# Optimization experiments

Measured on AMD Instinct MI355X. Metric: run time of the kernel, lower is better.

Reference implementation:

```python
import jax, jax.numpy as jnp
import numpy as np

NHEAD = 8
HEAD_DIM = 32  # per-head dim d; C = NHEAD * HEAD_DIM = 256
NEG_INF = -1e9


def setup_inputs() -> dict:
    key = jax.random.key(0)
    k1, k2, k3, k4, k5 = jax.random.split(key, 5)
    B, L, C = 8, 1024, NHEAD * HEAD_DIM
    query = jax.random.normal(k1, (B, L, C), dtype=jnp.float32)
    key_t = jax.random.normal(k2, (B, L, C), dtype=jnp.float32)
    value = jax.random.normal(k3, (B, L, C), dtype=jnp.float32)
    hard_mask = jax.random.randint(k4, (B, L), 0, 2).astype(bool)
    bias = jax.random.normal(k5, (B, L, L), dtype=jnp.float32)
    return {"query": query, "key": key_t, "value": value,
            "hard_mask": hard_mask, "bias": bias}


def reference(query, key, value, hard_mask, bias):
    # Faithful to the hard-mask path: attention is computed only among
    # active tokens (hard_mask True); inactive positions pass `value` through.
    # Masking inactive KEYS with -inf in the softmax is mathematically
    # identical to the sort/gather/slice/SDPA/scatter-unsort in the original.
    B, L, C = query.shape
    H, D = NHEAD, HEAD_DIM
    scale = 1.0 / jnp.sqrt(jnp.asarray(D, query.dtype))

    def split_heads(t):  # (B, L, C) -> (B, H, L, D)
        return t.reshape(B, L, H, D).transpose(0, 2, 1, 3)

    q, k, v = split_heads(query), split_heads(key), split_heads(value)

    # scores: (B, H, Lq, Lk); bias broadcasts over heads
    scores = jnp.einsum('bhld,bhmd->bhlm', q, k) * scale + bias[:, None, :, :]
    scores = jnp.where(hard_mask[:, None, None, :], scores, NEG_INF)
    attn = jax.nn.softmax(scores, axis=-1)
    out = jnp.einsum('bhlm,bhmd->bhld', attn, v)          # (B, H, L, D)
    out = out.transpose(0, 2, 1, 3).reshape(B, L, C)      # (B, L, C)

    # inactive query positions return the raw value (scatter-back behavior)
    out = jnp.where(hard_mask[:, :, None], out, value)

    # torch.stack over per-item (1, L, C) results -> (B, 1, L, C)
    return out[:, None, :, :]
```

## Files before the change

### kernel.cpp

```cpp
#include <hip/hip_runtime.h>
#include <hip/hip_bf16.h>

#define B_    8
#define H_    8
#define L_    1024
#define D_    32
#define C_    256
#define NK    64
#define PSTR  72

typedef __attribute__((ext_vector_type(8))) short bf16x8;
typedef __attribute__((ext_vector_type(4))) float f32x4;

__device__ inline unsigned short f2bf(float f) {
    union { float f; unsigned int u; } x; x.f = f;
    return (unsigned short)((x.u + 0x7fffu + ((x.u >> 16) & 1u)) >> 16);
}

__device__ inline unsigned int pk_bf16(float lo, float hi) {
    union { __hip_bfloat162 h; unsigned int u; } c;
    c.h = __float22bfloat162_rn(make_float2(lo, hi));
    return c.u;
}

__global__ __launch_bounds__(256) void prep_all(
    const float* __restrict__ k, const float* __restrict__ v,
    const float* __restrict__ bias, const int* __restrict__ mask,
    unsigned short* __restrict__ kfrag, unsigned short* __restrict__ vfrag,
    unsigned short* __restrict__ bfrag)
{
    const int tid = threadIdx.x;
    const int blk = blockIdx.x;
    __shared__ float sKf[64 * 36];
    __shared__ float sVf[64 * 33];
    __shared__ float sMadd[L_];

    if (blk < 1024) {
        const int bh = blk >> 4, c = blk & 15;
        const int b = bh >> 3, h = bh & 7;
        {
            const int row = tid >> 2, seg = tid & 3;
            const size_t src = (size_t)(b * L_ + c * 64 + row) * C_ + h * D_ + seg * 8;
            float4 a = *(const float4*)(k + src);
            float4 d = *(const float4*)(k + src + 4);
            *(float4*)(sKf + row * 36 + seg * 8) = a;
            *(float4*)(sKf + row * 36 + seg * 8 + 4) = d;
            float4 va = *(const float4*)(v + src);
            float4 vd = *(const float4*)(v + src + 4);
            float* vr = sVf + row * 33 + seg * 8;
            vr[0] = va.x; vr[1] = va.y; vr[2] = va.z; vr[3] = va.w;
            vr[4] = vd.x; vr[5] = vd.y; vr[6] = vd.z; vr[7] = vd.w;
        }
        __syncthreads();
        const int ln = tid & 63, u = tid >> 6;
        const int l16 = ln & 15, quad = ln >> 4;
        {
            const float* src = sKf + (u * 16 + l16) * 36 + quad * 8;
            float4 a = *(const float4*)src;
            float4 d = *(const float4*)(src + 4);
            uint4 o = { pk_bf16(a.x, a.y), pk_bf16(a.z, a.w),
                        pk_bf16(d.x, d.y), pk_bf16(d.z, d.w) };
            *(uint4*)(kfrag + (size_t)blk * 2048 + u * 512 + ln * 8) = o;
        }
        {
            const int s2 = u >> 1, nt = u & 1;
            float vals[8];
#pragma unroll
            for (int j = 0; j < 8; ++j)
                vals[j] = sVf[(s2 * 32 + quad * 8 + j) * 33 + nt * 16 + l16];
            uint4 o = { pk_bf16(vals[0], vals[1]), pk_bf16(vals[2], vals[3]),
                        pk_bf16(vals[4], vals[5]), pk_bf16(vals[6], vals[7]) };
            *(uint4*)(vfrag + (size_t)blk * 2048 + s2 * 1024 + nt * 512 + ln * 8) = o;
        }
    } else {
        const int bblk = blk - 1024;
        const int b = bblk >> 6, strip = bblk & 63;
        const int wv = tid >> 6, ln = tid & 63;
        const int l16 = ln & 15, quad = ln >> 4;
        {
            int4 m = ((const int4*)(mask + b * L_))[tid];
            sMadd[tid * 4 + 0] = m.x ? 0.f : -1e9f;
            sMadd[tid * 4 + 1] = m.y ? 0.f : -1e9f;
            sMadd[tid * 4 + 2] = m.z ? 0.f : -1e9f;
            sMadd[tid * 4 + 3] = m.w ? 0.f : -1e9f;
        }
        __syncthreads();
        const float* brow = bias + ((size_t)(b * L_) + strip * 16 + quad * 4) * L_;
        unsigned short* obase = bfrag + (size_t)bblk * 16384;
#pragma unroll
        for (int cc = 0; cc < 4; ++cc) {
            const int c = wv * 4 + cc;
            float vals[16];
#pragma unroll
            for (int nt = 0; nt < 4; ++nt) {
                const int col = c * 64 + nt * 16 + l16;
                const float madd = sMadd[col];
#pragma unroll
                for (int r = 0; r < 4; ++r)
                    vals[nt * 4 + r] = brow[(size_t)r * L_ + col] + madd;
            }
            uint4 o0 = { pk_bf16(vals[0],  vals[1]),  pk_bf16(vals[2],  vals[3]),
                         pk_bf16(vals[4],  vals[5]),  pk_bf16(vals[6],  vals[7]) };
            uint4 o1 = { pk_bf16(vals[8],  vals[9]),  pk_bf16(vals[10], vals[11]),
                         pk_bf16(vals[12], vals[13]), pk_bf16(vals[14], vals[15]) };
            *(uint4*)(obase + c * 1024 +   0 + ln * 8) = o0;
            *(uint4*)(obase + c * 1024 + 512 + ln * 8) = o1;
        }
    }
}

__global__ __launch_bounds__(256, 4) void attn_fa2(
    const float* __restrict__ q,
    const float* __restrict__ v,
    const int*   __restrict__ mask,
    const unsigned short* __restrict__ kfrag,
    const unsigned short* __restrict__ vfrag,
    const unsigned short* __restrict__ bfrag,
    float*       __restrict__ out)
{
    __shared__ __align__(16) unsigned short sP[4][16 * PSTR];

    const int tid  = threadIdx.x;
    const int wv   = tid >> 6;
    const int ln   = tid & 63;
    const int l16  = ln & 15;
    const int quad = ln >> 4;

    const int blk = blockIdx.x;
    const int h   = blk >> 7;
    const int rem = blk & 127;
    const int b   = rem >> 4;
    const int qt  = rem & 15;
    const int strip = qt * 4 + wv;
    const int q0  = strip * 16;
    const int bh  = b * H_ + h;

    const float scale = 0.17677669529663687f;

    bf16x8 qfrag;
    {
        const float* qp = q + ((size_t)(b * L_ + q0 + l16) * C_ + h * D_ + quad * 8);
        float4 a = ((const float4*)qp)[0];
        float4 c = ((const float4*)qp)[1];
        __align__(16) unsigned int u[4] = {
            pk_bf16(a.x * scale, a.y * scale), pk_bf16(a.z * scale, a.w * scale),
            pk_bf16(c.x * scale, c.y * scale), pk_bf16(c.z * scale, c.w * scale)};
        qfrag = *(const bf16x8*)u;
    }

    bf16x8 onesf;
#pragma unroll
    for (int i = 0; i < 8; ++i) onesf[i] = (short)0x3F80;

    const unsigned short* kf_base = kfrag + (size_t)bh * 32768 + ln * 8;
    const unsigned short* vf_base = vfrag + (size_t)bh * 32768 + ln * 8;
    const unsigned short* bm_base = bfrag + (size_t)(b * 64 + strip) * 16384 + ln * 8;
    unsigned short* const sPw = &sP[wv][0];

    f32x4 Oacc[2] = {{0.f,0.f,0.f,0.f},{0.f,0.f,0.f,0.f}};
    f32x4 Lacc    = {0.f,0.f,0.f,0.f};

    bf16x8 kf[4];
    uint4  bm[2];
#pragma unroll
    for (int nt = 0; nt < 4; ++nt)
        kf[nt] = *(const bf16x8*)(kf_base + nt * 512);
    bm[0] = *(const uint4*)(bm_base);
    bm[1] = *(const uint4*)(bm_base + 512);

    for (int c = 0; c < 16; ++c) {
        bf16x8 vf[4];
#pragma unroll
        for (int u2 = 0; u2 < 4; ++u2)
            vf[u2] = *(const bf16x8*)(vf_base + c * 2048 + u2 * 512);

        f32x4 S[4];
#pragma unroll
        for (int nt = 0; nt < 4; ++nt)
            S[nt] = __builtin_amdgcn_mfma_f32_16x16x32_bf16(
                qfrag, kf[nt], (f32x4){0.f,0.f,0.f,0.f}, 0, 0, 0);

        const int cn = (c < 15) ? c + 1 : 15;
        bf16x8 kfN[4];
        uint4  bmN[2];
#pragma unroll
        for (int nt = 0; nt < 4; ++nt)
            kfN[nt] = *(const bf16x8*)(kf_base + cn * 2048 + nt * 512);
        bmN[0] = *(const uint4*)(bm_base + cn * 1024);
        bmN[1] = *(const uint4*)(bm_base + cn * 1024 + 512);

        unsigned short* dst0 = sPw + quad * 4 * PSTR + l16;
#pragma unroll
        for (int nt = 0; nt < 4; ++nt) {
            const unsigned int w0 = ((const unsigned int*)&bm[nt >> 1])[(nt & 1) * 2 + 0];
            const unsigned int w1 = ((const unsigned int*)&bm[nt >> 1])[(nt & 1) * 2 + 1];
            const float b0 = __uint_as_float(w0 << 16);
            const float b1 = __uint_as_float(w0 & 0xffff0000u);
            const float b2 = __uint_as_float(w1 << 16);
            const float b3 = __uint_as_float(w1 & 0xffff0000u);
            const float p0 = __expf(S[nt][0] + b0);
            const float p1 = __expf(S[nt][1] + b1);
            const float p2 = __expf(S[nt][2] + b2);
            const float p3 = __expf(S[nt][3] + b3);
            const unsigned int plo = pk_bf16(p0, p1);
            const unsigned int phi = pk_bf16(p2, p3);
            unsigned short* d = dst0 + nt * 16;
            d[0 * PSTR] = (unsigned short)plo;
            d[1 * PSTR] = (unsigned short)(plo >> 16);
            d[2 * PSTR] = (unsigned short)phi;
            d[3 * PSTR] = (unsigned short)(phi >> 16);
        }

#pragma unroll
        for (int s2 = 0; s2 < 2; ++s2) {
            bf16x8 pf = *(const bf16x8*)(sPw + l16 * PSTR + s2 * 32 + quad * 8);
            Lacc = __builtin_amdgcn_mfma_f32_16x16x32_bf16(pf, onesf, Lacc, 0, 0, 0);
            Oacc[0] = __builtin_amdgcn_mfma_f32_16x16x32_bf16(pf, vf[s2 * 2 + 0], Oacc[0], 0, 0, 0);
            Oacc[1] = __builtin_amdgcn_mfma_f32_16x16x32_bf16(pf, vf[s2 * 2 + 1], Oacc[1], 0, 0, 0);
        }

#pragma unroll
        for (int nt = 0; nt < 4; ++nt) kf[nt] = kfN[nt];
        bm[0] = bmN[0];
        bm[1] = bmN[1];
    }

#pragma unroll
    for (int r = 0; r < 4; ++r) {
        const int qrow = q0 + quad * 4 + r;
        const int active = mask[b * L_ + qrow];
        const float inv = 1.f / Lacc[r];
        const size_t base = (size_t)(b * L_ + qrow) * C_ + h * D_;
#pragma unroll
        for (int nt = 0; nt < 2; ++nt) {
            const size_t idx = base + nt * 16 + l16;
            out[idx] = active ? Oacc[nt][r] * inv : v[idx];
        }
    }
}

#define MQ    64
#define KSTR  48
#define VSTR  72

__global__ __launch_bounds__(256) void masked_attn_mfma(
    const float* __restrict__ q,
    const float* __restrict__ k,
    const float* __restrict__ v,
    const int*   __restrict__ mask,
    const float* __restrict__ bias,
    float*       __restrict__ out)
{
    __shared__ __align__(16) unsigned short sQ[MQ][KSTR];
    __shared__ __align__(16) unsigned short sKt[NK][KSTR];
    __shared__ __align__(16) unsigned short sVt[D_][VSTR];
    __shared__ __align__(16) unsigned short sP2[4][16][VSTR];
    __shared__ float sMadd2[NK];

    const int tid  = threadIdx.x;
    const int wv   = tid >> 6;
    const int ln   = tid & 63;
    const int l16  = ln & 15;
    const int quad = ln >> 4;

    const int blk = blockIdx.x;
    const int h   = blk & 7;
    const int qt  = (blk >> 3) & 15;
    const int b   = blk >> 7;
    const int q0  = qt * MQ;
    const float scale = 0.17677669529663687f;

    {
        const int row = tid >> 2, d0 = (tid & 3) * 8;
        const float* src = q + ((size_t)(b * L_ + q0 + row) * C_ + h * D_ + d0);
        float4 a = ((const float4*)src)[0];
        float4 c = ((const float4*)src)[1];
        __align__(16) unsigned short t8[8] = {
            f2bf(a.x), f2bf(a.y), f2bf(a.z), f2bf(a.w),
            f2bf(c.x), f2bf(c.y), f2bf(c.z), f2bf(c.w)};
        *(int4*)&sQ[row][d0] = *(const int4*)t8;
    }
    __syncthreads();

    const bf16x8 qfrag = *(const bf16x8*)&sQ[wv * 16 + l16][quad * 8];
    f32x4 Oacc[2] = {{0.f,0.f,0.f,0.f},{0.f,0.f,0.f,0.f}};
    float lsum[4] = {0.f, 0.f, 0.f, 0.f};

    for (int j0 = 0; j0 < L_; j0 += NK) {
        __syncthreads();
        {
            const int row = tid >> 2, d0 = (tid & 3) * 8;
            const size_t src = (size_t)(b * L_ + j0 + row) * C_ + h * D_ + d0;
            float4 ka = ((const float4*)(k + src))[0];
            float4 kb = ((const float4*)(k + src))[1];
            __align__(16) unsigned short t8[8] = {
                f2bf(ka.x), f2bf(ka.y), f2bf(ka.z), f2bf(ka.w),
                f2bf(kb.x), f2bf(kb.y), f2bf(kb.z), f2bf(kb.w)};
            *(int4*)&sKt[row][d0] = *(const int4*)t8;

            float4 va = ((const float4*)(v + src))[0];
            float4 vb = ((const float4*)(v + src))[1];
            sVt[d0 + 0][row] = f2bf(va.x);
            sVt[d0 + 1][row] = f2bf(va.y);
            sVt[d0 + 2][row] = f2bf(va.z);
            sVt[d0 + 3][row] = f2bf(va.w);
            sVt[d0 + 4][row] = f2bf(vb.x);
            sVt[d0 + 5][row] = f2bf(vb.y);
            sVt[d0 + 6][row] = f2bf(vb.z);
            sVt[d0 + 7][row] = f2bf(vb.w);
            if (tid < NK) sMadd2[tid] = mask[b * L_ + j0 + tid] ? 0.f : -1e9f;
        }
        __syncthreads();

        bf16x8 kf[4];
#pragma unroll
        for (int nt = 0; nt < 4; ++nt)
            kf[nt] = *(const bf16x8*)&sKt[nt * 16 + l16][quad * 8];

        f32x4 S[4];
#pragma unroll
        for (int nt = 0; nt < 4; ++nt)
            S[nt] = __builtin_amdgcn_mfma_f32_16x16x32_bf16(
                qfrag, kf[nt], (f32x4){0.f,0.f,0.f,0.f}, 0, 0, 0);

        float psum[4] = {0.f, 0.f, 0.f, 0.f};
        const size_t brow0 = (size_t)(b * L_ + q0 + wv * 16 + quad * 4) * L_ + j0;
#pragma unroll
        for (int nt = 0; nt < 4; ++nt) {
            const float madd = sMadd2[nt * 16 + l16];
#pragma unroll
            for (int r = 0; r < 4; ++r) {
                float s = S[nt][r] * scale + bias[brow0 + (size_t)r * L_ + nt * 16 + l16] + madd;
                float p = __expf(s);
                psum[r] += p;
                S[nt][r] = p;
            }
        }
#pragma unroll
        for (int nt = 0; nt < 4; ++nt)
#pragma unroll
            for (int r = 0; r < 4; ++r)
                sP2[wv][quad * 4 + r][nt * 16 + l16] = f2bf(S[nt][r]);
#pragma unroll
        for (int r = 0; r < 4; ++r) {
            float t = psum[r];
            t += __shfl_xor(t, 1);
            t += __shfl_xor(t, 2);
            t += __shfl_xor(t, 4);
            t += __shfl_xor(t, 8);
            lsum[r] += t;
        }
#pragma unroll
        for (int s2 = 0; s2 < 2; ++s2) {
            bf16x8 pf = *(const bf16x8*)&sP2[wv][l16][s2 * 32 + quad * 8];
#pragma unroll
            for (int nt = 0; nt < 2; ++nt) {
                bf16x8 vf = *(const bf16x8*)&sVt[nt * 16 + l16][s2 * 32 + quad * 8];
                Oacc[nt] = __builtin_amdgcn_mfma_f32_16x16x32_bf16(pf, vf, Oacc[nt], 0, 0, 0);
            }
        }
    }
#pragma unroll
    for (int r = 0; r < 4; ++r) {
        const int qg = q0 + wv * 16 + quad * 4 + r;
        const int active = mask[b * L_ + qg];
        const size_t obase = (size_t)(b * L_ + qg) * C_ + h * D_;
        const float inv = 1.f / lsum[r];
#pragma unroll
        for (int nt = 0; nt < 2; ++nt) {
            float val;
            if (active) val = Oacc[nt][r] * inv;
            else        val = v[obase + nt * 16 + l16];
            out[obase + nt * 16 + l16] = val;
        }
    }
}

extern "C" void kernel_launch(void* const* d_in, const int* in_sizes, int n_in,
                              void* d_out, int out_size, void* d_ws, size_t ws_size,
                              hipStream_t stream) {
    const float* q    = (const float*)d_in[0];
    const float* k    = (const float*)d_in[1];
    const float* v    = (const float*)d_in[2];
    const int*   mask = (const int*)d_in[3];
    const float* bias = (const float*)d_in[4];
    float* out = (float*)d_out;

    if (ws_size >= (size_t)24 * 1024 * 1024) {
        unsigned short* kfrag = (unsigned short*)d_ws;
        unsigned short* vfrag = kfrag + (size_t)2 * 1024 * 1024;
        unsigned short* bfrag = vfrag + (size_t)2 * 1024 * 1024;
        prep_all<<<1536, 256, 0, stream>>>(k, v, bias, mask, kfrag, vfrag, bfrag);
        attn_fa2<<<1024, 256, 0, stream>>>(q, v, mask, kfrag, vfrag, bfrag, out);
    } else {
        masked_attn_mfma<<<1024, 256, 0, stream>>>(q, k, v, mask, bias, out);
    }
}
```

Baseline: 127.3 us.

## Transpose score MFMA and bias fragment layout for coalesced bias reads and vector P stores

Swaps the MFMA operands so each lane holds four consecutive keys of one query row instead of four rows of one key. The bias prep now reads float4-contiguous bias rows and writes them in a matching transposed bf16 fragment layout. The attention kernel can then store each P fragment as one 8-byte LDS write instead of four scalar 2-byte writes. The intent is to cut LDS store instructions and improve coalescing of the large bias read, at the cost of a different bank access pattern on the P writes.

After: 130.5 us. 2.5% more time.

```diff
diff --git a/kernel.cpp b/kernel.cpp
--- a/kernel.cpp
+++ b/kernel.cpp
@@ -27,7 +27,7 @@
     const float* __restrict__ k, const float* __restrict__ v,
     const float* __restrict__ bias, const int* __restrict__ mask,
     unsigned short* __restrict__ kfrag, unsigned short* __restrict__ vfrag,
-    unsigned short* __restrict__ bfrag)
+    unsigned short* __restrict__ bfragT)
 {
     const int tid = threadIdx.x;
     const int blk = blockIdx.x;
@@ -75,8 +75,6 @@
     } else {
         const int bblk = blk - 1024;
         const int b = bblk >> 6, strip = bblk & 63;
-        const int wv = tid >> 6, ln = tid & 63;
-        const int l16 = ln & 15, quad = ln >> 4;
         {
             int4 m = ((const int4*)(mask + b * L_))[tid];
             sMadd[tid * 4 + 0] = m.x ? 0.f : -1e9f;
@@ -85,37 +83,30 @@
             sMadd[tid * 4 + 3] = m.w ? 0.f : -1e9f;
         }
         __syncthreads();
-        const float* brow = bias + ((size_t)(b * L_) + strip * 16 + quad * 4) * L_;
-        unsigned short* obase = bfrag + (size_t)bblk * 16384;
-#pragma unroll
-        for (int cc = 0; cc < 4; ++cc) {
-            const int c = wv * 4 + cc;
-            float vals[16];
-#pragma unroll
-            for (int nt = 0; nt < 4; ++nt) {
-                const int col = c * 64 + nt * 16 + l16;
-                const float madd = sMadd[col];
-#pragma unroll
-                for (int r = 0; r < 4; ++r)
-                    vals[nt * 4 + r] = brow[(size_t)r * L_ + col] + madd;
-            }
-            uint4 o0 = { pk_bf16(vals[0],  vals[1]),  pk_bf16(vals[2],  vals[3]),
-                         pk_bf16(vals[4],  vals[5]),  pk_bf16(vals[6],  vals[7]) };
-            uint4 o1 = { pk_bf16(vals[8],  vals[9]),  pk_bf16(vals[10], vals[11]),
-                         pk_bf16(vals[12], vals[13]), pk_bf16(vals[14], vals[15]) };
-            *(uint4*)(obase + c * 1024 +   0 + ln * 8) = o0;
-            *(uint4*)(obase + c * 1024 + 512 + ln * 8) = o1;
-        }
-    }
-}
-
-__global__ __launch_bounds__(256, 4) void attn_fa2(
+        const int l16 = tid >> 4, ntp = (tid >> 2) & 3, qp = tid & 3;
+        const float* brow = bias + ((size_t)(b * L_) + strip * 16 + l16) * L_;
+        unsigned short* obase = bfragT + (size_t)bblk * 16384
+                                + (qp * 16 + l16) * 16 + ntp * 4;
+        const int koff = ntp * 16 + qp * 4;
+#pragma unroll 4
+        for (int c = 0; c < 16; ++c) {
+            const int key = c * 64 + koff;
+            float4 a = *(const float4*)(brow + key);
+            const float* mp = sMadd + key;
+            uint2 o = { pk_bf16(a.x + mp[0], a.y + mp[1]),
+                        pk_bf16(a.z + mp[2], a.w + mp[3]) };
+            *(uint2*)(obase + c * 1024) = o;
+        }
+    }
+}
+
+__global__ __launch_bounds__(256, 4) void attn_fa3(
     const float* __restrict__ q,
     const float* __restrict__ v,
     const int*   __restrict__ mask,
     const unsigned short* __restrict__ kfrag,
     const unsigned short* __restrict__ vfrag,
-    const unsigned short* __restrict__ bfrag,
+    const unsigned short* __restrict__ bfragT,
     float*       __restrict__ out)
 {
     __shared__ __align__(16) unsigned short sP[4][16 * PSTR];
@@ -152,9 +143,9 @@
 #pragma unroll
     for (int i = 0; i < 8; ++i) onesf[i] = (short)0x3F80;
 
-    const unsigned short* kf_base = kfrag + (size_t)bh * 32768 + ln * 8;
-    const unsigned short* vf_base = vfrag + (size_t)bh * 32768 + ln * 8;
-    const unsigned short* bm_base = bfrag + (size_t)(b * 64 + strip) * 16384 + ln * 8;
+    const unsigned short* kf_base = kfrag  + (size_t)bh * 32768 + ln * 8;
+    const unsigned short* vf_base = vfrag  + (size_t)bh * 32768 + ln * 8;
+    const unsigned short* bm_base = bfragT + (size_t)(b * 64 + strip) * 16384 + ln * 16;
     unsigned short* const sPw = &sP[wv][0];
 
     f32x4 Oacc[2] = {{0.f,0.f,0.f,0.f},{0.f,0.f,0.f,0.f}};
@@ -166,7 +157,7 @@
     for (int nt = 0; nt < 4; ++nt)
         kf[nt] = *(const bf16x8*)(kf_base + nt * 512);
     bm[0] = *(const uint4*)(bm_base);
-    bm[1] = *(const uint4*)(bm_base + 512);
+    bm[1] = *(const uint4*)(bm_base + 8);
 
     for (int c = 0; c < 16; ++c) {
         bf16x8 vf[4];
@@ -178,7 +169,7 @@
 #pragma unroll
         for (int nt = 0; nt < 4; ++nt)
             S[nt] = __builtin_amdgcn_mfma_f32_16x16x32_bf16(
-                qfrag, kf[nt], (f32x4){0.f,0.f,0.f,0.f}, 0, 0, 0);
+                kf[nt], qfrag, (f32x4){0.f,0.f,0.f,0.f}, 0, 0, 0);
 
         const int cn = (c < 15) ? c + 1 : 15;
         bf16x8 kfN[4];
@@ -187,13 +178,13 @@
         for (int nt = 0; nt < 4; ++nt)
             kfN[nt] = *(const bf16x8*)(kf_base + cn * 2048 + nt * 512);
         bmN[0] = *(const uint4*)(bm_base + cn * 1024);
-        bmN[1] = *(const uint4*)(bm_base + cn * 1024 + 512);
-
-        unsigned short* dst0 = sPw + quad * 4 * PSTR + l16;
+        bmN[1] = *(const uint4*)(bm_base + cn * 1024 + 8);
+
+        unsigned short* const prow = sPw + l16 * PSTR + quad * 4;
 #pragma unroll
         for (int nt = 0; nt < 4; ++nt) {
-            const unsigned int w0 = ((const unsigned int*)&bm[nt >> 1])[(nt & 1) * 2 + 0];
-            const unsigned int w1 = ((const unsigned int*)&bm[nt >> 1])[(nt & 1) * 2 + 1];
+            const unsigned int w0 = ((const unsigned int*)bm)[2 * nt];
+            const unsigned int w1 = ((const unsigned int*)bm)[2 * nt + 1];
             const float b0 = __uint_as_float(w0 << 16);
             const float b1 = __uint_as_float(w0 & 0xffff0000u);
             const float b2 = __uint_as_float(w1 << 16);
@@ -202,13 +193,8 @@
             const float p1 = __expf(S[nt][1] + b1);
             const float p2 = __expf(S[nt][2] + b2);
             const float p3 = __expf(S[nt][3] + b3);
-            const unsigned int plo = pk_bf16(p0, p1);
-            const unsigned int phi = pk_bf16(p2, p3);
-            unsigned short* d = dst0 + nt * 16;
-            d[0 * PSTR] = (unsigned short)plo;
-            d[1 * PSTR] = (unsigned short)(plo >> 16);
-            d[2 * PSTR] = (unsigned short)phi;
-            d[3 * PSTR] = (unsigned short)(phi >> 16);
+            uint2 pw = { pk_bf16(p0, p1), pk_bf16(p2, p3) };
+            *(uint2*)(prow + nt * 16) = pw;
         }
 
 #pragma unroll
@@ -387,11 +373,11 @@
     float* out = (float*)d_out;
 
     if (ws_size >= (size_t)24 * 1024 * 1024) {
-        unsigned short* kfrag = (unsigned short*)d_ws;
-        unsigned short* vfrag = kfrag + (size_t)2 * 1024 * 1024;
-        unsigned short* bfrag = vfrag + (size_t)2 * 1024 * 1024;
-        prep_all<<<1536, 256, 0, stream>>>(k, v, bias, mask, kfrag, vfrag, bfrag);
-        attn_fa2<<<1024, 256, 0, stream>>>(q, v, mask, kfrag, vfrag, bfrag, out);
+        unsigned short* kfrag  = (unsigned short*)d_ws;
+        unsigned short* vfrag  = kfrag + (size_t)2 * 1024 * 1024;
+        unsigned short* bfragT = vfrag + (size_t)2 * 1024 * 1024;
+        prep_all<<<1536, 256, 0, stream>>>(k, v, bias, mask, kfrag, vfrag, bfragT);
+        attn_fa3<<<1024, 256, 0, stream>>>(q, v, mask, kfrag, vfrag, bfragT, out);
     } else {
         masked_attn_mfma<<<1024, 256, 0, stream>>>(q, k, v, mask, bias, out);
     }
```
